# Kernel optimization log

Hardware: AMD Instinct MI355X
Metric: run time of the kernel (lower is better)

Reference implementation:

```python
import jax, jax.numpy as jnp
import numpy as np

B, T, M = 32, 14, 2048
Q_DIM, KV_DIM, H = 768, 1024, 12
HD = Q_DIM // H
FF = 4 * Q_DIM
EPS = 1e-5


def layer_norm(x, g, b):
    mu = jnp.mean(x, axis=-1, keepdims=True)
    var = jnp.var(x, axis=-1, keepdims=True)
    return (x - mu) / jnp.sqrt(var + EPS) * g + b


def setup_inputs() -> dict:
    key = jax.random.key(0)
    ks = jax.random.split(key, 12)
    s = 0.02
    return {
        "expert_tokens": jax.random.normal(ks[0], (B, T, Q_DIM), jnp.float32),
        "key_value_embeddings": jax.random.normal(ks[1], (B, M, KV_DIM), jnp.float32),
        # per-expert-token query projections (stacked W_Q_list)
        "WQ": jax.random.normal(ks[2], (T, Q_DIM, Q_DIM), jnp.float32) * s,
        "bQ": jnp.zeros((T, Q_DIM), jnp.float32),
        "WK": jax.random.normal(ks[3], (KV_DIM, Q_DIM), jnp.float32) * s,
        "bK": jnp.zeros((Q_DIM,), jnp.float32),
        "WV": jax.random.normal(ks[4], (KV_DIM, Q_DIM), jnp.float32) * s,
        "bV": jnp.zeros((Q_DIM,), jnp.float32),
        "W1": jax.random.normal(ks[5], (Q_DIM, FF), jnp.float32) * s,
        "b1": jnp.zeros((FF,), jnp.float32),
        "W2": jax.random.normal(ks[6], (FF, Q_DIM), jnp.float32) * s,
        "b2": jnp.zeros((Q_DIM,), jnp.float32),
        "g1": jnp.ones((Q_DIM,), jnp.float32),
        "be1": jnp.zeros((Q_DIM,), jnp.float32),
        "g2": jnp.ones((Q_DIM,), jnp.float32),
        "be2": jnp.zeros((Q_DIM,), jnp.float32),
    }


def reference(expert_tokens, key_value_embeddings, WQ, bQ, WK, bK, WV, bV,
              W1, b1, W2, b2, g1, be1, g2, be2):
    b_, t_, e_ = expert_tokens.shape
    m_ = key_value_embeddings.shape[1]
    # Batched grouped projection: distinct W_Q per expert token (replaces the python loop)
    Q = (jnp.einsum('bte,teq->btq', expert_tokens, WQ) + bQ).reshape(b_, t_, H, HD)
    K = (key_value_embeddings @ WK + bK).reshape(b_, m_, H, HD)
    V = (key_value_embeddings @ WV + bV).reshape(b_, m_, H, HD)
    scale = jnp.sqrt(jnp.asarray(HD, jnp.float32))
    scores = jnp.einsum('bthd,bmhd->bthm', Q, K) / scale
    attn_w = jax.nn.softmax(scores, axis=-1)  # [B,T,H,M]; dropout is identity at eval
    attn_out = jnp.einsum('bthm,bmhd->bthd', attn_w, V).reshape(b_, t_, e_)
    x = layer_norm(expert_tokens + attn_out, g1, be1)
    ff = jnp.maximum(x @ W1 + b1, 0.0) @ W2 + b2
    out = layer_norm(x + ff, g2, be2)
    return out, attn_w
```

## Files before the change

kernel.cpp:

```cpp
#include <hip/hip_runtime.h>
#include <cstdint>
#include <cstddef>

#define BBATCH 32
#define TT 14
#define MM 2048
#define QD 768
#define NHEAD 12
#define HD 64
#define FFD 3072
#define KVD 1024

typedef short bf16x8 __attribute__((ext_vector_type(8)));
typedef float f32x4 __attribute__((ext_vector_type(4)));

__device__ __forceinline__ uint16_t f2b(float f) {
  union { float f; uint32_t u; } v; v.f = f;
  uint32_t r = v.u + 0x7fffu + ((v.u >> 16) & 1u);
  return (uint16_t)(r >> 16);
}
__device__ __forceinline__ float b2f(uint16_t b) {
  union { uint32_t u; float f; } v; v.u = ((uint32_t)b) << 16; return v.f;
}

__device__ __forceinline__ void glds16(const void* g, void* l) {
  __builtin_amdgcn_global_load_lds(
      (const __attribute__((address_space(1))) void*)g,
      (__attribute__((address_space(3))) void*)l, 16, 0, 0);
}

__global__ void k_cast8(const float4* __restrict__ in, uint4* __restrict__ out) {
  int i = blockIdx.x * blockDim.x + threadIdx.x;
  float4 a = in[2 * i], b = in[2 * i + 1];
  uint4 o;
  o.x = (uint32_t)f2b(a.x) | ((uint32_t)f2b(a.y) << 16);
  o.y = (uint32_t)f2b(a.z) | ((uint32_t)f2b(a.w) << 16);
  o.z = (uint32_t)f2b(b.x) | ((uint32_t)f2b(b.y) << 16);
  o.w = (uint32_t)f2b(b.z) | ((uint32_t)f2b(b.w) << 16);
  out[i] = o;
}

__global__ void k_transpose_bf16(const float* __restrict__ in, uint16_t* __restrict__ out,
                                 int R, int C) {
  __shared__ float tile[32][33];
  int bz = blockIdx.z;
  int c0 = blockIdx.x * 32, r0 = blockIdx.y * 32;
  int tx = threadIdx.x & 31, ty = threadIdx.x >> 5;
  const float* inb = in + (size_t)bz * R * C;
  uint16_t* outb = out + (size_t)bz * R * C;
#pragma unroll
  for (int rr = 0; rr < 32; rr += 8)
    tile[ty + rr][tx] = inb[(size_t)(r0 + ty + rr) * C + c0 + tx];
  __syncthreads();
#pragma unroll
  for (int rr = 0; rr < 32; rr += 8)
    outb[(size_t)(c0 + ty + rr) * R + r0 + tx] = f2b(tile[tx][ty + rr]);
}

__global__ void k_bias_concat(const float* __restrict__ bK, const float* __restrict__ bV,
                              float* __restrict__ out) {
  int i = blockIdx.x * 256 + threadIdx.x;
  out[i] = (i < QD) ? bK[i] : bV[i - QD];
}

__global__ __launch_bounds__(256, 2) void k_gemm_kv(
    const uint16_t* __restrict__ A, const uint16_t* __restrict__ Bt,
    const float* __restrict__ bias, uint16_t* __restrict__ Kh, uint16_t* __restrict__ Vt) {
  __shared__ __align__(16) uint16_t As[3 * 4096];
  __shared__ __align__(16) uint16_t Bs[3 * 8192];
  const int K = KVD;
  int tid = threadIdx.x;
  int w = tid >> 6, l = tid & 63;

  int wgid = blockIdx.y * 6 + blockIdx.x;
  int swz = (wgid & 7) * 384 + (wgid >> 3);
  int bx = swz % 6, by = swz / 6;
  int m0 = by * 128, n0 = bx * 256;
  int wm = (w >> 1) * 64, wn = (w & 1) * 128;

  f32x4 zero4 = {0.f, 0.f, 0.f, 0.f};
  f32x4 acc[4][8];
#pragma unroll
  for (int i = 0; i < 4; i++)
#pragma unroll
    for (int j = 0; j < 8; j++) acc[i][j] = zero4;

  int sr = tid >> 2;
  int xs8 = (((tid & 3) ^ ((tid >> 3) & 3))) * 8;
  const uint16_t* gA0 = A + (size_t)(m0 + sr) * K + xs8;
  const uint16_t* gA1 = A + (size_t)(m0 + 64 + sr) * K + xs8;
  const uint16_t* gB0 = Bt + (size_t)(n0 + sr) * K + xs8;
  const uint16_t* gB1 = Bt + (size_t)(n0 + 64 + sr) * K + xs8;
  const uint16_t* gB2 = Bt + (size_t)(n0 + 128 + sr) * K + xs8;
  const uint16_t* gB3 = Bt + (size_t)(n0 + 192 + sr) * K + xs8;

  int lm = l & 15, q = l >> 4;
  int qp = (q ^ ((lm >> 1) & 3)) * 8;

  auto stage = [&](int buf, int kt) {
    uint16_t* a = As + buf * 4096 + w * 512;
    uint16_t* b = Bs + buf * 8192 + w * 512;
    glds16(gA0 + kt, a);
    glds16(gA1 + kt, a + 2048);
    glds16(gB0 + kt, b);
    glds16(gB1 + kt, b + 2048);
    glds16(gB2 + kt, b + 4096);
    glds16(gB3 + kt, b + 6144);
  };
  auto compute = [&](int buf) {
    const uint16_t* as = As + buf * 4096;
    const uint16_t* bs = Bs + buf * 8192;
    bf16x8 af[4], bfv[8];
#pragma unroll
    for (int i = 0; i < 4; i++)
      af[i] = *(const bf16x8*)&as[(wm + i * 16 + lm) * 32 + qp];
#pragma unroll
    for (int j = 0; j < 8; j++)
      bfv[j] = *(const bf16x8*)&bs[(wn + j * 16 + lm) * 32 + qp];
#pragma unroll
    for (int i = 0; i < 4; i++)
#pragma unroll
      for (int j = 0; j < 8; j++)
        acc[i][j] = __builtin_amdgcn_mfma_f32_16x16x32_bf16(af[i], bfv[j], acc[i][j], 0, 0, 0);
  };

  const int NT = K / 32;
  stage(0, 0);
  stage(1, 32);
  int cur = 0;
  for (int t = 0; t < NT - 1; ++t) {
    asm volatile("s_waitcnt vmcnt(6)" ::: "memory");
    __builtin_amdgcn_s_barrier();
    if (t + 2 < NT) {
      int sb = cur + 2; if (sb >= 3) sb -= 3;
      stage(sb, (t + 2) * 32);
    }
    compute(cur);
    cur = (cur == 2) ? 0 : cur + 1;
  }
  asm volatile("s_waitcnt vmcnt(0)" ::: "memory");
  __builtin_amdgcn_s_barrier();
  compute(cur);

#pragma unroll
  for (int j = 0; j < 8; j++) {
    int col = n0 + wn + j * 16 + lm;
    float bc = bias[col];
    bool isV = col >= QD;
    int c2 = isV ? col - QD : col;
    int h = c2 >> 6, d = c2 & 63;
#pragma unroll
    for (int i = 0; i < 4; i++) {
      int rowb = m0 + wm + i * 16 + q * 4;
#pragma unroll
      for (int r = 0; r < 4; r++) {
        int row = rowb + r;
        int b = row >> 11, m = row & 2047;
        float v = acc[i][j][r] + bc;
        if (isV)
          Vt[((((size_t)b * NHEAD + h) * HD) + d) * MM + m] = f2b(v);
        else
          Kh[(((size_t)b * NHEAD + h) * MM + m) * HD + d] = f2b(v);
      }
    }
  }
}

template <bool RELU, bool OUTF32>
__global__ __launch_bounds__(256) void k_gemm64(
    const uint16_t* __restrict__ A, const uint16_t* __restrict__ Bt,
    const float* __restrict__ bias, void* __restrict__ Cv, int K, int N) {
  __shared__ __align__(16) uint16_t As[3 * 2048];
  __shared__ __align__(16) uint16_t Bs[3 * 2048];
  int tid = threadIdx.x;
  int w = tid >> 6, l = tid & 63;
  int m0 = blockIdx.y * 64, n0 = blockIdx.x * 64;
  int wm = (w >> 1) * 32, wn = (w & 1) * 32;
  f32x4 zero4 = {0.f, 0.f, 0.f, 0.f};
  f32x4 acc[2][2];
#pragma unroll
  for (int i = 0; i < 2; i++)
#pragma unroll
    for (int j = 0; j < 2; j++) acc[i][j] = zero4;

  int sr = tid >> 2;
  int xs8 = (((tid & 3) ^ ((tid >> 3) & 3))) * 8;
  const uint16_t* gA = A + (size_t)(m0 + sr) * K + xs8;
  const uint16_t* gB = Bt + (size_t)(n0 + sr) * K + xs8;
  int lm = l & 15, q = l >> 4;
  int qp = (q ^ ((lm >> 1) & 3)) * 8;

  auto stage = [&](int buf, int kt) {
    glds16(gA + kt, As + buf * 2048 + w * 512);
    glds16(gB + kt, Bs + buf * 2048 + w * 512);
  };
  auto compute = [&](int buf) {
    const uint16_t* as = As + buf * 2048;
    const uint16_t* bs = Bs + buf * 2048;
    bf16x8 af[2], bfv[2];
#pragma unroll
    for (int i = 0; i < 2; i++) {
      af[i] = *(const bf16x8*)&as[(wm + i * 16 + lm) * 32 + qp];
      bfv[i] = *(const bf16x8*)&bs[(wn + i * 16 + lm) * 32 + qp];
    }
#pragma unroll
    for (int i = 0; i < 2; i++)
#pragma unroll
      for (int j = 0; j < 2; j++)
        acc[i][j] = __builtin_amdgcn_mfma_f32_16x16x32_bf16(af[i], bfv[j], acc[i][j], 0, 0, 0);
  };

  const int NT = K / 32;
  stage(0, 0);
  stage(1, 32);
  int cur = 0;
  for (int t = 0; t < NT - 1; ++t) {
    asm volatile("s_waitcnt vmcnt(2)" ::: "memory");
    __builtin_amdgcn_s_barrier();
    if (t + 2 < NT) {
      int sb = cur + 2; if (sb >= 3) sb -= 3;
      stage(sb, (t + 2) * 32);
    }
    compute(cur);
    cur = (cur == 2) ? 0 : cur + 1;
  }
  asm volatile("s_waitcnt vmcnt(0)" ::: "memory");
  __builtin_amdgcn_s_barrier();
  compute(cur);

#pragma unroll
  for (int j = 0; j < 2; j++) {
    int col = n0 + wn + j * 16 + lm;
    float bc = bias[col];
#pragma unroll
    for (int i = 0; i < 2; i++) {
      int rowb = m0 + wm + i * 16 + q * 4;
#pragma unroll
      for (int r = 0; r < 4; r++) {
        float v = acc[i][j][r] + bc;
        if (RELU) v = fmaxf(v, 0.f);
        if (OUTF32)
          ((float*)Cv)[(size_t)(rowb + r) * N + col] = v;
        else
          ((uint16_t*)Cv)[(size_t)(rowb + r) * N + col] = f2b(v);
      }
    }
  }
}

__global__ __launch_bounds__(256) void k_gemm_q(
    const uint16_t* __restrict__ Xb, const uint16_t* __restrict__ WQt,
    const float* __restrict__ bQ, float* __restrict__ Q) {
  __shared__ __align__(16) uint16_t As[32 * 32];
  __shared__ __align__(16) uint16_t Bs[64 * 32];
  int tid = threadIdx.x;
  int w = tid >> 6, l = tid & 63;
  int t = blockIdx.y, n0 = blockIdx.x * 64;
  const uint16_t* Wt = WQt + (size_t)t * QD * QD;
  f32x4 zero4 = {0.f, 0.f, 0.f, 0.f};
  f32x4 acc[2] = {zero4, zero4};
  int sr = tid >> 2;
  int xs8 = (((tid & 3) ^ ((tid >> 3) & 3))) * 8;
  const uint16_t* gA = Xb + ((size_t)(sr * TT + t)) * QD + xs8;
  const uint16_t* gB = Wt + (size_t)(n0 + sr) * QD + xs8;
  int lm = l & 15, q = l >> 4;
  int qp = (q ^ ((lm >> 1) & 3)) * 8;
  for (int kt = 0; kt < QD; kt += 32) {
    __syncthreads();
    if (tid < 128) glds16(gA + kt, As + w * 512);
    glds16(gB + kt, Bs + w * 512);
    __syncthreads();
    bf16x8 bfv = *(const bf16x8*)&Bs[(w * 16 + lm) * 32 + qp];
#pragma unroll
    for (int i = 0; i < 2; i++) {
      bf16x8 af = *(const bf16x8*)&As[(i * 16 + lm) * 32 + qp];
      acc[i] = __builtin_amdgcn_mfma_f32_16x16x32_bf16(af, bfv, acc[i], 0, 0, 0);
    }
  }
  int col = n0 + w * 16 + lm;
  float bc = bQ[t * QD + col];
#pragma unroll
  for (int i = 0; i < 2; i++) {
    int b0 = i * 16 + q * 4;
#pragma unroll
    for (int r = 0; r < 4; r++) {
      int b = b0 + r;
      Q[((size_t)(b * TT + t)) * QD + col] = acc[i][r] + bc;
    }
  }
}

__global__ __launch_bounds__(256) void k_scores(
    const float* __restrict__ Q,
    const uint16_t* __restrict__ Kh,
    float* __restrict__ AW) {
  __shared__ __align__(16) float Qs[7][64];
  __shared__ float redv[4];
  int tid = threadIdx.x;
  int tg = blockIdx.x, h = blockIdx.y, b = blockIdx.z;
  int t0 = tg * 7;
  for (int i = tid; i < 7 * 64; i += 256) {
    int t = i >> 6, d = i & 63;
    Qs[t][d] = Q[((size_t)(b * TT + t0 + t)) * QD + h * HD + d] * 0.125f;
  }
  __syncthreads();
  float acc[7][8];
#pragma unroll
  for (int t = 0; t < 7; t++)
#pragma unroll
    for (int c = 0; c < 8; c++) acc[t][c] = 0.f;

  const uint16_t* kb = Kh + ((size_t)(b * NHEAD + h)) * MM * HD;
  for (int c = 0; c < 8; c++) {
    const uint16_t* kr = kb + (size_t)(c * 256 + tid) * HD;
#pragma unroll
    for (int dv = 0; dv < 8; dv++) {
      uint4 u = *(const uint4*)(kr + dv * 8);
      float kf[8];
      kf[0] = __uint_as_float(u.x << 16); kf[1] = __uint_as_float(u.x & 0xffff0000u);
      kf[2] = __uint_as_float(u.y << 16); kf[3] = __uint_as_float(u.y & 0xffff0000u);
      kf[4] = __uint_as_float(u.z << 16); kf[5] = __uint_as_float(u.z & 0xffff0000u);
      kf[6] = __uint_as_float(u.w << 16); kf[7] = __uint_as_float(u.w & 0xffff0000u);
#pragma unroll
      for (int t = 0; t < 7; t++) {
        float4 qa = *(const float4*)&Qs[t][dv * 8];
        float4 qb = *(const float4*)&Qs[t][dv * 8 + 4];
        float s = acc[t][c];
        s = fmaf(kf[0], qa.x, s); s = fmaf(kf[1], qa.y, s);
        s = fmaf(kf[2], qa.z, s); s = fmaf(kf[3], qa.w, s);
        s = fmaf(kf[4], qb.x, s); s = fmaf(kf[5], qb.y, s);
        s = fmaf(kf[6], qb.z, s); s = fmaf(kf[7], qb.w, s);
        acc[t][c] = s;
      }
    }
  }
  int lane = tid & 63, w = tid >> 6;
#pragma unroll
  for (int t = 0; t < 7; t++) {
    float mx = acc[t][0];
#pragma unroll
    for (int c = 1; c < 8; c++) mx = fmaxf(mx, acc[t][c]);
#pragma unroll
    for (int o = 32; o > 0; o >>= 1) mx = fmaxf(mx, __shfl_xor(mx, o));
    if (lane == 0) redv[w] = mx;
    __syncthreads();
    mx = fmaxf(fmaxf(redv[0], redv[1]), fmaxf(redv[2], redv[3]));
    __syncthreads();
    float s = 0.f;
#pragma unroll
    for (int c = 0; c < 8; c++) {
      float e = __expf(acc[t][c] - mx);
      acc[t][c] = e;
      s += e;
    }
#pragma unroll
    for (int o = 32; o > 0; o >>= 1) s += __shfl_xor(s, o);
    if (lane == 0) redv[w] = s;
    __syncthreads();
    s = redv[0] + redv[1] + redv[2] + redv[3];
    __syncthreads();
    float inv = 1.f / s;
    size_t rowb = ((size_t)((b * TT + t0 + t) * NHEAD + h)) * MM;
#pragma unroll
    for (int c = 0; c < 8; c++) AW[rowb + c * 256 + tid] = acc[t][c] * inv;
  }
}

__global__ __launch_bounds__(256) void k_attnout(
    const float* __restrict__ AW, const uint16_t* __restrict__ Vt,
    float* __restrict__ AO) {
  int tid = threadIdx.x;
  int h = blockIdx.x, b = blockIdx.y;
  int d = tid & 63, tg = tid >> 6;
  const uint16_t* vr = Vt + (((size_t)(b * NHEAD + h)) * HD + d) * MM;
  const float* pb = AW + ((size_t)(b * TT * NHEAD + h)) * MM;
  float acc[4] = {0.f, 0.f, 0.f, 0.f};
#pragma unroll 2
  for (int mc = 0; mc < MM; mc += 8) {
    uint4 u = *(const uint4*)(vr + mc);
    float vf[8];
    vf[0] = __uint_as_float(u.x << 16); vf[1] = __uint_as_float(u.x & 0xffff0000u);
    vf[2] = __uint_as_float(u.y << 16); vf[3] = __uint_as_float(u.y & 0xffff0000u);
    vf[4] = __uint_as_float(u.z << 16); vf[5] = __uint_as_float(u.z & 0xffff0000u);
    vf[6] = __uint_as_float(u.w << 16); vf[7] = __uint_as_float(u.w & 0xffff0000u);
#pragma unroll
    for (int i = 0; i < 4; i++) {
      int t = tg * 4 + i;
      if (t < TT) {
        const float* pr = pb + (size_t)t * NHEAD * MM + mc;
        float4 p0 = *(const float4*)pr;
        float4 p1 = *(const float4*)(pr + 4);
        float s = acc[i];
        s = fmaf(vf[0], p0.x, s); s = fmaf(vf[1], p0.y, s);
        s = fmaf(vf[2], p0.z, s); s = fmaf(vf[3], p0.w, s);
        s = fmaf(vf[4], p1.x, s); s = fmaf(vf[5], p1.y, s);
        s = fmaf(vf[6], p1.z, s); s = fmaf(vf[7], p1.w, s);
        acc[i] = s;
      }
    }
  }
#pragma unroll
  for (int i = 0; i < 4; i++) {
    int t = tg * 4 + i;
    if (t < TT) AO[((size_t)(b * TT + t)) * QD + h * HD + d] = acc[i];
  }
}

__global__ __launch_bounds__(256) void k_add_ln(
    const float* __restrict__ X, const float* __restrict__ Y,
    const float* __restrict__ g, const float* __restrict__ be,
    float* __restrict__ outF, uint16_t* __restrict__ outB) {
  __shared__ float redS[4], redQ[4];
  int r = blockIdx.x, tid = threadIdx.x;
  size_t base = (size_t)r * QD;
  float e[3];
  float s = 0.f, sq = 0.f;
#pragma unroll
  for (int j = 0; j < 3; j++) {
    float v = X[base + tid + j * 256] + Y[base + tid + j * 256];
    e[j] = v; s += v; sq += v * v;
  }
#pragma unroll
  for (int o = 32; o > 0; o >>= 1) { s += __shfl_xor(s, o); sq += __shfl_xor(sq, o); }
  if ((tid & 63) == 0) { redS[tid >> 6] = s; redQ[tid >> 6] = sq; }
  __syncthreads();
  s = redS[0] + redS[1] + redS[2] + redS[3];
  sq = redQ[0] + redQ[1] + redQ[2] + redQ[3];
  float mu = s * (1.f / QD);
  float var = sq * (1.f / QD) - mu * mu;
  float rstd = rsqrtf(var + 1e-5f);
#pragma unroll
  for (int j = 0; j < 3; j++) {
    int i = tid + j * 256;
    float v = (e[j] - mu) * rstd * g[i] + be[i];
    outF[base + i] = v;
    if (outB) outB[base + i] = f2b(v);
  }
}

extern "C" void kernel_launch(void* const* d_in, const int* in_sizes, int n_in,
                              void* d_out, int out_size, void* d_ws, size_t ws_size,
                              hipStream_t stream) {
  const float* tok = (const float*)d_in[0];
  const float* kve = (const float*)d_in[1];
  const float* WQ  = (const float*)d_in[2];
  const float* bQ  = (const float*)d_in[3];
  const float* WK  = (const float*)d_in[4];
  const float* bK  = (const float*)d_in[5];
  const float* WV  = (const float*)d_in[6];
  const float* bV  = (const float*)d_in[7];
  const float* W1  = (const float*)d_in[8];
  const float* b1  = (const float*)d_in[9];
  const float* W2  = (const float*)d_in[10];
  const float* b2  = (const float*)d_in[11];
  const float* g1  = (const float*)d_in[12];
  const float* be1 = (const float*)d_in[13];
  const float* g2  = (const float*)d_in[14];
  const float* be2 = (const float*)d_in[15];

  float* outp = (float*)d_out;
  float* AW = outp + 448 * 768;

  char* p = (char*)d_ws;
  auto nxt = [&](size_t bytes) -> char* {
    char* r = p;
    p += (bytes + 255) & ~(size_t)255;
    return r;
  };
  uint16_t* Abf   = (uint16_t*)nxt((size_t)67108864 * 2);
  uint16_t* Kh    = (uint16_t*)nxt((size_t)50331648 * 2);
  uint16_t* Vt    = (uint16_t*)nxt((size_t)50331648 * 2);
  uint16_t* Wkvt  = (uint16_t*)nxt((size_t)1572864 * 2);
  uint16_t* WQt   = (uint16_t*)nxt((size_t)8257536 * 2);
  uint16_t* W1t   = (uint16_t*)nxt((size_t)2359296 * 2);
  uint16_t* W2t   = (uint16_t*)nxt((size_t)2359296 * 2);
  uint16_t* xtokb = (uint16_t*)nxt((size_t)344064 * 2);
  float* biaskv   = (float*)nxt(1536 * 4);
  float* Qws      = (float*)nxt((size_t)344064 * 4);
  float* AOws     = (float*)nxt((size_t)344064 * 4);
  float* xws      = (float*)nxt((size_t)344064 * 4);
  uint16_t* xbf   = (uint16_t*)nxt((size_t)344064 * 2);
  uint16_t* h1bf  = (uint16_t*)nxt((size_t)1376256 * 2);
  float* yws      = (float*)nxt((size_t)344064 * 4);

  k_cast8<<<dim3(32768), dim3(256), 0, stream>>>((const float4*)kve, (uint4*)Abf);
  k_cast8<<<dim3(168), dim3(256), 0, stream>>>((const float4*)tok, (uint4*)xtokb);
  k_transpose_bf16<<<dim3(24, 32, 1), dim3(256), 0, stream>>>(WK, Wkvt, 1024, 768);
  k_transpose_bf16<<<dim3(24, 32, 1), dim3(256), 0, stream>>>(WV, Wkvt + (size_t)768 * 1024, 1024, 768);
  k_transpose_bf16<<<dim3(24, 24, 14), dim3(256), 0, stream>>>(WQ, WQt, 768, 768);
  k_transpose_bf16<<<dim3(96, 24, 1), dim3(256), 0, stream>>>(W1, W1t, 768, 3072);
  k_transpose_bf16<<<dim3(24, 96, 1), dim3(256), 0, stream>>>(W2, W2t, 3072, 768);
  k_bias_concat<<<dim3(6), dim3(256), 0, stream>>>(bK, bV, biaskv);

  k_gemm_kv<<<dim3(6, 512), dim3(256), 0, stream>>>(Abf, Wkvt, biaskv, Kh, Vt);

  k_gemm_q<<<dim3(12, 14), dim3(256), 0, stream>>>(xtokb, WQt, bQ, Qws);

  k_scores<<<dim3(2, 12, 32), dim3(256), 0, stream>>>(Qws, Kh, AW);

  k_attnout<<<dim3(12, 32), dim3(256), 0, stream>>>(AW, Vt, AOws);

  k_add_ln<<<dim3(448), dim3(256), 0, stream>>>(tok, AOws, g1, be1, xws, xbf);

  k_gemm64<true, false><<<dim3(48, 7), dim3(256), 0, stream>>>(xbf, W1t, b1, (void*)h1bf, 768, 3072);
  k_gemm64<false, true><<<dim3(12, 7), dim3(256), 0, stream>>>(h1bf, W2t, b2, (void*)yws, 3072, 768);

  k_add_ln<<<dim3(448), dim3(256), 0, stream>>>(xws, yws, g2, be2, outp, (uint16_t*)nullptr);
}
```

Baseline: 1.403 ms.

## Split attention-output reduction over M into 8 chunks, reduce partials in LayerNorm

The attention-output kernel previously launched only 384 blocks, each walking the full 2048-length key dimension serially. It now splits M into 8 chunks of 256 via a third grid dimension and writes partial sums to a per-chunk buffer. The following add+LayerNorm kernel, now templated on the chunk count, sums those partials. This raises parallelism on a latency-bound phase at the cost of extra partial-buffer traffic, about 11 MB written and then read back.

```diff
diff --git a/kernel.cpp b/kernel.cpp
--- a/kernel.cpp
+++ b/kernel.cpp
@@ -10,6 +10,8 @@
 #define HD 64
 #define FFD 3072
 #define KVD 1024
+#define ROWS 448
+#define CHSTRIDE 344064
 
 typedef short bf16x8 __attribute__((ext_vector_type(8)));
 typedef float f32x4 __attribute__((ext_vector_type(4)));
@@ -368,16 +370,17 @@
 
 __global__ __launch_bounds__(256) void k_attnout(
     const float* __restrict__ AW, const uint16_t* __restrict__ Vt,
-    float* __restrict__ AO) {
+    float* __restrict__ pbuf) {
   int tid = threadIdx.x;
-  int h = blockIdx.x, b = blockIdx.y;
+  int h = blockIdx.x, b = blockIdx.y, mc = blockIdx.z;
   int d = tid & 63, tg = tid >> 6;
-  const uint16_t* vr = Vt + (((size_t)(b * NHEAD + h)) * HD + d) * MM;
-  const float* pb = AW + ((size_t)(b * TT * NHEAD + h)) * MM;
+  int m0 = mc * 256;
+  const uint16_t* vr = Vt + (((size_t)(b * NHEAD + h)) * HD + d) * MM + m0;
+  const float* pb = AW + ((size_t)(b * TT * NHEAD + h)) * MM + m0;
   float acc[4] = {0.f, 0.f, 0.f, 0.f};
 #pragma unroll 2
-  for (int mc = 0; mc < MM; mc += 8) {
-    uint4 u = *(const uint4*)(vr + mc);
+  for (int mcc = 0; mcc < 256; mcc += 8) {
+    uint4 u = *(const uint4*)(vr + mcc);
     float vf[8];
     vf[0] = __uint_as_float(u.x << 16); vf[1] = __uint_as_float(u.x & 0xffff0000u);
     vf[2] = __uint_as_float(u.y << 16); vf[3] = __uint_as_float(u.y & 0xffff0000u);
@@ -387,7 +390,7 @@
     for (int i = 0; i < 4; i++) {
       int t = tg * 4 + i;
       if (t < TT) {
-        const float* pr = pb + (size_t)t * NHEAD * MM + mc;
+        const float* pr = pb + (size_t)t * NHEAD * MM + mcc;
         float4 p0 = *(const float4*)pr;
         float4 p1 = *(const float4*)(pr + 4);
         float s = acc[i];
@@ -402,12 +405,14 @@
 #pragma unroll
   for (int i = 0; i < 4; i++) {
     int t = tg * 4 + i;
-    if (t < TT) AO[((size_t)(b * TT + t)) * QD + h * HD + d] = acc[i];
-  }
-}
-
+    if (t < TT)
+      pbuf[(size_t)mc * CHSTRIDE + ((size_t)(b * TT + t)) * QD + h * HD + d] = acc[i];
+  }
+}
+
+template <int NCHUNK>
 __global__ __launch_bounds__(256) void k_add_ln(
-    const float* __restrict__ X, const float* __restrict__ Y,
+    const float* __restrict__ X, const float* __restrict__ P,
     const float* __restrict__ g, const float* __restrict__ be,
     float* __restrict__ outF, uint16_t* __restrict__ outB) {
   __shared__ float redS[4], redQ[4];
@@ -417,7 +422,10 @@
   float s = 0.f, sq = 0.f;
 #pragma unroll
   for (int j = 0; j < 3; j++) {
-    float v = X[base + tid + j * 256] + Y[base + tid + j * 256];
+    int i = tid + j * 256;
+    float v = X[base + i];
+#pragma unroll
+    for (int c = 0; c < NCHUNK; c++) v += P[(size_t)c * CHSTRIDE + base + i];
     e[j] = v; s += v; sq += v * v;
   }
 #pragma unroll
@@ -477,7 +485,7 @@
   uint16_t* xtokb = (uint16_t*)nxt((size_t)344064 * 2);
   float* biaskv   = (float*)nxt(1536 * 4);
   float* Qws      = (float*)nxt((size_t)344064 * 4);
-  float* AOws     = (float*)nxt((size_t)344064 * 4);
+  float* pbuf     = (float*)nxt((size_t)8 * CHSTRIDE * 4);
   float* xws      = (float*)nxt((size_t)344064 * 4);
   uint16_t* xbf   = (uint16_t*)nxt((size_t)344064 * 2);
   uint16_t* h1bf  = (uint16_t*)nxt((size_t)1376256 * 2);
@@ -498,12 +506,12 @@
 
   k_scores<<<dim3(2, 12, 32), dim3(256), 0, stream>>>(Qws, Kh, AW);
 
-  k_attnout<<<dim3(12, 32), dim3(256), 0, stream>>>(AW, Vt, AOws);
-
-  k_add_ln<<<dim3(448), dim3(256), 0, stream>>>(tok, AOws, g1, be1, xws, xbf);
+  k_attnout<<<dim3(12, 32, 8), dim3(256), 0, stream>>>(AW, Vt, pbuf);
+
+  k_add_ln<8><<<dim3(448), dim3(256), 0, stream>>>(tok, pbuf, g1, be1, xws, xbf);
 
   k_gemm64<true, false><<<dim3(48, 7), dim3(256), 0, stream>>>(xbf, W1t, b1, (void*)h1bf, 768, 3072);
   k_gemm64<false, true><<<dim3(12, 7), dim3(256), 0, stream>>>(h1bf, W2t, b2, (void*)yws, 3072, 768);
 
-  k_add_ln<<<dim3(448), dim3(256), 0, stream>>>(xws, yws, g2, be2, outp, (uint16_t*)nullptr);
-}
+  k_add_ln<1><<<dim3(448), dim3(256), 0, stream>>>(xws, yws, g2, be2, outp, (uint16_t*)nullptr);
+}
```

Measured after the change: 1.224 ms. 1.15x faster.
